# Kernel optimization log

Hardware: AMD Instinct MI355X
Metric: run time of the kernel (lower is better)

## Reference

```python
import jax, jax.numpy as jnp
import numpy as np

KS = 3      # kernel_size
PAD = 1     # zero padding applied to x before sampling
STRIDE = 1  # stride of p_conv and final conv (as written in the repo)


def conv2d(x, w, b=None, stride=1, padding=0):
    out = jax.lax.conv_general_dilated(
        x, w, (stride, stride), [(padding, padding), (padding, padding)],
        dimension_numbers=("NCHW", "OIHW", "NCHW"))
    if b is not None:
        out = out + b[None, :, None, None]
    return out


def setup_inputs() -> dict:
    key = jax.random.key(0)
    k1, k2, k3, k4 = jax.random.split(key, 4)
    bsz, inc, outc, H, W = 4, 64, 128, 128, 128
    N = KS * KS
    x = jax.random.normal(k1, (bsz, inc, H, W), dtype=jnp.float32)
    # p_conv: Conv2d(inc, 2*ks*ks, 3, padding=1) with bias (small weights -> modest offsets)
    w_p = jax.random.normal(k2, (2 * N, inc, 3, 3), dtype=jnp.float32) * 0.02
    b_p = jax.random.normal(k3, (2 * N,), dtype=jnp.float32) * 0.1
    # final conv: Conv2d(inc, outc, ks, stride=stride, bias=None)
    w_conv = jax.random.normal(k4, (outc, inc, KS, KS), dtype=jnp.float32) * 0.05
    return {"x": x, "w_p": w_p, "b_p": b_p, "w_conv": w_conv}


def deform_conv_forward(x, w_p, b_p, w_conv):
    ks, pad, stride = KS, PAD, STRIDE
    offset = conv2d(x, w_p, b_p, stride=stride, padding=1)  # (b, 2N, oh, ow)
    N = offset.shape[1] // 2
    bsz, c, _, _ = x.shape
    oh, ow = offset.shape[2], offset.shape[3]
    xp = jnp.pad(x, ((0, 0), (0, 0), (pad, pad), (pad, pad)))
    Hp, Wp = xp.shape[2], xp.shape[3]

    # p_n: kernel-grid offsets, order matches torch.meshgrid 'ij' then flatten
    r = jnp.arange(-(ks - 1) // 2, (ks - 1) // 2 + 1, dtype=x.dtype)
    pnx, pny = jnp.meshgrid(r, r, indexing="ij")
    p_n = jnp.concatenate([pnx.ravel(), pny.ravel()])[None, :, None, None]  # (1,2N,1,1)

    # p_0: base sampling coordinates (1-indexed into padded image)
    i0 = jnp.arange(1, oh * stride + 1, stride, dtype=x.dtype)
    j0 = jnp.arange(1, ow * stride + 1, stride, dtype=x.dtype)
    p0x = jnp.broadcast_to(i0[:, None], (oh, ow))[None, None]
    p0y = jnp.broadcast_to(j0[None, :], (oh, ow))[None, None]
    p_0 = jnp.concatenate([jnp.tile(p0x, (1, N, 1, 1)), jnp.tile(p0y, (1, N, 1, 1))], axis=1)

    p = (p_0 + p_n + offset).transpose(0, 2, 3, 1)  # (b, oh, ow, 2N)

    q_lt_f = jnp.floor(p)
    q_rb_f = q_lt_f + 1.0

    def clamp_q(q):
        return jnp.concatenate(
            [jnp.clip(q[..., :N], 0, Hp - 1), jnp.clip(q[..., N:], 0, Wp - 1)],
            axis=-1).astype(jnp.int32)

    q_lt = clamp_q(q_lt_f)
    q_rb = clamp_q(q_rb_f)
    q_lb = jnp.concatenate([q_lt[..., :N], q_rb[..., N:]], axis=-1)
    q_rt = jnp.concatenate([q_rb[..., :N], q_lt[..., N:]], axis=-1)

    # clamp p itself (indices are detached in torch; gradients flow only through p here)
    p = jnp.concatenate(
        [jnp.clip(p[..., :N], 0, Hp - 1), jnp.clip(p[..., N:], 0, Wp - 1)], axis=-1)
    px, py = p[..., :N], p[..., N:]

    qf = lambda q: q.astype(x.dtype)
    g_lt = (1 + (qf(q_lt[..., :N]) - px)) * (1 + (qf(q_lt[..., N:]) - py))
    g_rb = (1 - (qf(q_rb[..., :N]) - px)) * (1 - (qf(q_rb[..., N:]) - py))
    g_lb = (1 + (qf(q_lb[..., :N]) - px)) * (1 - (qf(q_lb[..., N:]) - py))
    g_rt = (1 - (qf(q_rt[..., :N]) - px)) * (1 + (qf(q_rt[..., N:]) - py))

    x_flat = xp.reshape(bsz, c, Hp * Wp)

    def get_x_q(q):
        idx = q[..., :N] * Wp + q[..., N:]                     # (b, oh, ow, N)
        idxf = jnp.broadcast_to(idx.reshape(bsz, 1, -1), (bsz, c, oh * ow * N))
        return jnp.take_along_axis(x_flat, idxf, axis=2).reshape(bsz, c, oh, ow, N)

    x_off = (g_lt[:, None] * get_x_q(q_lt) + g_rb[:, None] * get_x_q(q_rb)
             + g_lb[:, None] * get_x_q(q_lb) + g_rt[:, None] * get_x_q(q_rt))

    # _reshape_x_offset: (b,c,oh,ow,ks*ks) -> (b,c,oh*ks,ow*ks)
    x_off = x_off.reshape(bsz, c, oh, ow, ks, ks).transpose(0, 1, 2, 4, 3, 5)
    x_off = x_off.reshape(bsz, c, oh * ks, ow * ks)

    return conv2d(x_off, w_conv, None, stride=stride, padding=0)


def reference(x, w_p, b_p, w_conv):
    return deform_conv_forward(x, w_p, b_p, w_conv)
```

## Files before the change

kernel.cpp:

```cpp
#include <hip/hip_runtime.h>
#include <hip/hip_bf16.h>

#define B_   4
#define IC   64
#define OC   128
#define HH   128
#define WW   128
#define HP   130
#define XOF  384
#define XPAD 388
#define OH2  382

typedef __attribute__((ext_vector_type(4))) float f32x4;
typedef __attribute__((ext_vector_type(8))) __bf16 bf16x8;
typedef __attribute__((ext_vector_type(8))) unsigned short us8;
typedef __attribute__((ext_vector_type(4), aligned(4))) float f32x4u;

__device__ __forceinline__ void gload16(const void* gsrc, void* ldst) {
    __builtin_amdgcn_global_load_lds(
        (const __attribute__((address_space(1))) void*)gsrc,
        (__attribute__((address_space(3))) void*)ldst, 16, 0, 0);
}

#define WAITV(N) asm volatile("s_waitcnt vmcnt(" #N ")" ::: "memory")

__device__ __forceinline__ float bf2f(unsigned short u) {
    union { unsigned int i; float f; } v; v.i = ((unsigned int)u) << 16; return v.f;
}
__device__ __forceinline__ unsigned short f2bf(float f) {
    __hip_bfloat16 h = __float2bfloat16(f);
    return reinterpret_cast<unsigned short&>(h);
}

__global__ __launch_bounds__(256) void prologue(const float* __restrict__ x,
                                                const float* __restrict__ w_p,
                                                const float* __restrict__ b_p,
                                                const float* __restrict__ wc,
                                                float* __restrict__ off,
                                                unsigned short* __restrict__ xt,
                                                unsigned short* __restrict__ Bt) {
    __shared__ __align__(16) char smem[18432];
    int bid = blockIdx.x;
    int tid = threadIdx.x;

    if (bid < 2048) {
        unsigned short (*tile)[34] = (unsigned short(*)[34])smem;
        int xt4 = bid & 3;
        int y   = (bid >> 2) & 127;
        int b   = bid >> 9;
        int x0  = xt4 * 32;

        int xl = tid & 31;
        int c8 = tid >> 5;
#pragma unroll
        for (int it = 0; it < 8; ++it) {
            int c = it * 8 + c8;
            tile[c][xl] = f2bf(x[(((size_t)b * IC + c) * HH + y) * WW + x0 + xl]);
        }
        __syncthreads();
        int c2 = (tid & 31) * 2;
#pragma unroll
        for (int it = 0; it < 4; ++it) {
            int xx = (tid >> 5) + it * 8;
            ushort2 v = { tile[c2][xx], tile[c2 + 1][xx] };
            *(ushort2*)(xt + (((size_t)b * HH + y) * WW + x0 + xx) * IC + c2) = v;
        }
    } else if (bid < 3072) {
        float (*part)[64][18] = (float(*)[64][18])smem;
        int obid = bid - 2048;
        int pxl = tid & 63;
        int icq = tid >> 6;
        int seg = obid & 1;
        int row = obid >> 1;
        int py  = row & 127;
        int b   = row >> 7;
        int px  = seg * 64 + pxl;
        int ic0 = __builtin_amdgcn_readfirstlane(icq << 4);

        float acc[18];
#pragma unroll
        for (int co = 0; co < 18; ++co) acc[co] = 0.f;

        const float* xb = x + ((size_t)b * IC + ic0) * HH * WW;

        for (int ci = 0; ci < 16; ++ci) {
            const float* xc = xb + (size_t)ci * HH * WW;
            float xv[9];
#pragma unroll
            for (int ky = 0; ky < 3; ++ky) {
                int yy = py + ky - 1;
                bool yok = (yy >= 0) && (yy < HH);
#pragma unroll
                for (int kx = 0; kx < 3; ++kx) {
                    int xx = px + kx - 1;
                    bool ok = yok && (xx >= 0) && (xx < WW);
                    xv[ky * 3 + kx] = ok ? xc[yy * WW + xx] : 0.f;
                }
            }
#pragma unroll
            for (int co = 0; co < 18; ++co) {
                const float* wrow = w_p + ((size_t)co * IC + ic0 + ci) * 9;
                f32x4u w0 = *(const f32x4u*)wrow;
                f32x4u w1 = *(const f32x4u*)(wrow + 4);
                float  w8 = wrow[8];
                acc[co] = fmaf(w0.x, xv[0], acc[co]);
                acc[co] = fmaf(w0.y, xv[1], acc[co]);
                acc[co] = fmaf(w0.z, xv[2], acc[co]);
                acc[co] = fmaf(w0.w, xv[3], acc[co]);
                acc[co] = fmaf(w1.x, xv[4], acc[co]);
                acc[co] = fmaf(w1.y, xv[5], acc[co]);
                acc[co] = fmaf(w1.z, xv[6], acc[co]);
                acc[co] = fmaf(w1.w, xv[7], acc[co]);
                acc[co] = fmaf(w8,   xv[8], acc[co]);
            }
        }

#pragma unroll
        for (int co = 0; co < 18; ++co) part[icq][pxl][co] = acc[co];
        __syncthreads();

        for (int co = icq; co < 18; co += 4) {
            float s = b_p[co] + part[0][pxl][co] + part[1][pxl][co]
                              + part[2][pxl][co] + part[3][pxl][co];
            off[((size_t)b * 18 + co) * HH * WW + (size_t)py * WW + px] = s;
        }
    } else {
        int t = (bid - 3072) * 256 + tid;
        if (t < 18 * 4 * 128 * 8) {
            int e  = t & 7;
            int oc = (t >> 3) & 127;
            int kg = (t >> 10) & 3;
            int s  = t >> 12;
            int ic = ((s & 1) << 5) + (kg << 3) + e;
            int kpos = s >> 1;
            int ky = kpos / 3, kx = kpos % 3;
            Bt[t] = f2bf(wc[(((size_t)oc * IC + ic) * 3 + ky) * 3 + kx]);
        }
    }
}

__global__ __launch_bounds__(256) void sample_nhwc(const unsigned short* __restrict__ xt,
                                                   const float* __restrict__ off,
                                                   unsigned short* __restrict__ xoff,
                                                   int b0, int nwg) {
    int orig = blockIdx.x;
    int chunk = nwg >> 3;
    int wg = (orig & 7) * chunk + (orig >> 3);

    int xtile = wg % 12;
    int tmp = wg / 12;
    int yy  = tmp % XOF;
    int bl  = tmp / XOF;
    int b   = b0 + bl;
    int xx0 = xtile * 32;

    int t  = threadIdx.x;
    int xl = t & 31;
    int cg = t >> 5;
    int xx = xx0 + xl;

    int j = xx / 3, kw = xx % 3;
    int i = yy / 3, kh = yy % 3;
    int n = kh * 3 + kw;

    const float* offb = off + (size_t)b * 18 * HH * WW + (size_t)i * WW + j;
    float offr = offb[(size_t)n * HH * WW];
    float offc = offb[(size_t)(n + 9) * HH * WW];

    float pr = (float)(i + kh) + offr;
    float pc = (float)(j + kw) + offc;

    float r0f = floorf(pr), c0f = floorf(pc);
    int r0 = min(max((int)r0f, 0), HP - 1);
    int c0 = min(max((int)c0f, 0), HP - 1);
    int r1 = min(max((int)(r0f + 1.f), 0), HP - 1);
    int c1 = min(max((int)(c0f + 1.f), 0), HP - 1);

    float prc = fminf(fmaxf(pr, 0.f), (float)(HP - 1));
    float pcc = fminf(fmaxf(pc, 0.f), (float)(HP - 1));

    float R0 = 1.f + ((float)r0 - prc);
    float R1 = 1.f - ((float)r1 - prc);
    float C0 = 1.f + ((float)c0 - pcc);
    float C1 = 1.f - ((float)c1 - pcc);

    int rr0 = r0 - 1, cc0 = c0 - 1, rr1 = r1 - 1, cc1 = c1 - 1;
    if (!(rr0 >= 0 && rr0 < HH)) R0 = 0.f;
    if (!(rr1 >= 0 && rr1 < HH)) R1 = 0.f;
    float C0m = (cc0 >= 0 && cc0 < WW) ? C0 : 0.f;
    float C1m = (cc1 >= 0 && cc1 < WW) ? C1 : 0.f;
    int ra0 = min(max(rr0, 0), HH - 1);
    int ra1 = min(max(rr1, 0), HH - 1);
    int ca0 = min(max(cc0, 0), WW - 1);
    int ca1 = min(max(cc1, 0), WW - 1);

    const unsigned short* xb = xt + (size_t)b * HH * WW * IC + cg * 8;
    us8 a  = *(const us8*)(xb + ((size_t)ra0 * WW + ca0) * IC);
    us8 bb = *(const us8*)(xb + ((size_t)ra0 * WW + ca1) * IC);
    us8 cc = *(const us8*)(xb + ((size_t)ra1 * WW + ca0) * IC);
    us8 dd = *(const us8*)(xb + ((size_t)ra1 * WW + ca1) * IC);

    us8 res;
#pragma unroll
    for (int e = 0; e < 8; ++e) {
        float v = R0 * (C0m * bf2f(a[e]) + C1m * bf2f(bb[e])) +
                  R1 * (C0m * bf2f(cc[e]) + C1m * bf2f(dd[e]));
        res[e] = f2bf(v);
    }

    size_t di = ((((size_t)bl * XOF + yy) * 8 + cg) * XPAD + xx) * 8;
    *(us8*)(xoff + di) = res;
}

__global__ __launch_bounds__(256) void conv2_mfma(const unsigned short* __restrict__ xoff,
                                                  const unsigned short* __restrict__ Bt,
                                                  float* __restrict__ out,
                                                  int b0, int nwg) {
    __shared__ __align__(16) char lds[49152];

    int orig = blockIdx.x;
    int q = nwg >> 3, r = nwg & 7;
    int xcd = orig & 7, loc = orig >> 3;
    int wgid = (xcd < r ? xcd * (q + 1) : r * (q + 1) + (xcd - r) * q) + loc;

    int xt  = wgid % 3;
    int tmp = wgid / 3;
    int oy  = tmp % OH2;
    int bl  = tmp / OH2;
    int x0  = xt << 7;

    int tid  = threadIdx.x;
    int wave = tid >> 6, lane = tid & 63;
    int wm = wave >> 1;
    int wn = wave & 1;
    int lr = lane & 15, lc = lane >> 4;

    const char* xb = (const char*)xoff + (size_t)bl * ((size_t)XOF * 8 * XPAD * 16);
    const char* bt = (const char*)Bt;

    f32x4 acc[4][4];
#pragma unroll
    for (int mf = 0; mf < 4; ++mf)
#pragma unroll
        for (int nf = 0; nf < 4; ++nf)
            acc[mf][nf] = (f32x4){0.f, 0.f, 0.f, 0.f};

    auto stageA_full = [&](int abuf, int s6) {
#pragma unroll
        for (int qq = 0; qq < 3; ++qq) {
            int ky  = s6 >> 1;
            int ich = s6 & 1;
            int L   = wave * 3 + qq;
            int cg  = L / 3, seg = L % 3;
            const char* src = xb +
                (((size_t)(oy + ky) * 8 + ich * 4 + cg) * XPAD + x0 + seg * 64 + lane) * 16;
            char* dst = lds + abuf * 12288 + (cg * 192 + seg * 64) * 16;
            gload16(src, dst);
        }
    };
    auto stageB = [&](int t) {
        int s6 = t / 3, kx = t % 3;
        int sB = ((s6 >> 1) * 3 + kx) * 2 + (s6 & 1);
        int buf = t % 3;
        const char* bsrc = bt + (size_t)sB * 8192;
#pragma unroll
        for (int g2 = 0; g2 < 2; ++g2) {
            int g = wave * 2 + g2;
            gload16(bsrc + (size_t)g * 1024 + lane * 16,
                    lds + 24576 + buf * 8192 + g * 1024);
        }
    };

    auto compute = [&](int abuf, int t, int kx) {
        const char* abase = lds + abuf * 12288;
        const char* bbase = lds + 24576 + (t % 3) * 8192;
        bf16x8 af[4], bfr[4];
#pragma unroll
        for (int mf = 0; mf < 4; ++mf)
            af[mf] = *(const bf16x8*)(abase +
                (lc * 192 + wm * 64 + mf * 16 + lr + kx) * 16);
#pragma unroll
        for (int nf = 0; nf < 4; ++nf)
            bfr[nf] = *(const bf16x8*)(bbase +
                (lc * 128 + wn * 64 + nf * 16 + lr) * 16);
        __builtin_amdgcn_s_setprio(1);
#pragma unroll
        for (int mf = 0; mf < 4; ++mf)
#pragma unroll
            for (int nf = 0; nf < 4; ++nf)
                acc[mf][nf] = __builtin_amdgcn_mfma_f32_16x16x32_bf16(
                    af[mf], bfr[nf], acc[mf][nf], 0, 0, 0);
        __builtin_amdgcn_s_setprio(0);
    };

    stageA_full(0, 0);
    stageB(0);
    stageB(1);

#pragma unroll
    for (int t = 0; t < 18; ++t) {
        const int kx = t % 3, s6 = t / 3;
        const int n = (t == 17) ? 0 : ((t % 3 == 1 && t < 15) ? 5 : 2);
        if (n == 0)      { WAITV(0); }
        else if (n == 2) { WAITV(2); }
        else             { WAITV(5); }
        __builtin_amdgcn_s_barrier();
        __builtin_amdgcn_sched_barrier(0);
        if (t + 2 < 18) stageB(t + 2);
        if (kx == 0 && s6 + 1 < 6) stageA_full((s6 & 1) ^ 1, s6 + 1);
        compute(s6 & 1, t, kx);
        __builtin_amdgcn_sched_barrier(0);
    }

    int b = b0 + bl;
#pragma unroll
    for (int mf = 0; mf < 4; ++mf) {
        int ox0 = x0 + wm * 64 + mf * 16 + (lc << 2);
#pragma unroll
        for (int nf = 0; nf < 4; ++nf) {
            int oc = wn * 64 + nf * 16 + lr;
            float* po = out + (((size_t)b * OC + oc) * OH2 + oy) * OH2 + ox0;
            if (ox0 + 3 < OH2) {
                *(f32x4u*)po = acc[mf][nf];
            } else {
#pragma unroll
                for (int rr = 0; rr < 4; ++rr)
                    if (ox0 + rr < OH2) po[rr] = acc[mf][nf][rr];
            }
        }
    }
}

extern "C" void kernel_launch(void* const* d_in, const int* in_sizes, int n_in,
                              void* d_out, int out_size, void* d_ws, size_t ws_size,
                              hipStream_t stream) {
    const float* x      = (const float*)d_in[0];
    const float* w_p    = (const float*)d_in[1];
    const float* b_p    = (const float*)d_in[2];
    const float* w_conv = (const float*)d_in[3];
    float* out = (float*)d_out;

    const size_t offElems = (size_t)B_ * 18 * HH * WW;
    const size_t xtElems  = (size_t)B_ * HH * WW * IC;
    const size_t btElems  = (size_t)18 * 4 * 128 * 8;
    const size_t xofElems = (size_t)XOF * 8 * XPAD * 8;
    const size_t slack    = 16384;

    float* off = (float*)d_ws;
    unsigned short* xtb  = (unsigned short*)(off + offElems);
    unsigned short* Bt   = xtb + xtElems;
    unsigned short* xoff = Bt + btElems;

    const size_t headBytes = offElems * 4 + (xtElems + btElems) * 2;
    const bool allBatch = ws_size >= headBytes + 4 * xofElems * 2 + slack;

    prologue<<<3360, 256, 0, stream>>>(x, w_p, b_p, w_conv, off, xtb, Bt);

    if (allBatch) {
        int snwg = 12 * XOF * B_;
        sample_nhwc<<<snwg, 256, 0, stream>>>(xtb, off, xoff, 0, snwg);
        int cnwg = 3 * OH2 * B_;
        conv2_mfma<<<cnwg, 256, 0, stream>>>(xoff, Bt, out, 0, cnwg);
    } else {
        for (int b = 0; b < B_; ++b) {
            int snwg = 12 * XOF;
            sample_nhwc<<<snwg, 256, 0, stream>>>(xtb, off, xoff, b, snwg);
            int cnwg = 3 * OH2;
            conv2_mfma<<<cnwg, 256, 0, stream>>>(xoff, Bt, out, b, cnwg);
        }
    }
}
```

Baseline: 217.7 us.

## Load conv weights straight to registers and cut per-step LDS barriers

The B (weight) fragments are now loaded from global memory directly into double-buffered registers, instead of being staged through LDS with async global-to-LDS copies. LDS now holds only the double-buffered A tile, with a padded row stride of 194, which shrinks LDS use. The workgroup barrier now runs only when the A buffer switches, once every three k-steps, rather than on every step. This trades shared weight staging for redundant per-wave global/L2 reads of the weights, in exchange for fewer barriers, less LDS traffic and possibly higher occupancy.

```diff
diff --git a/kernel.cpp b/kernel.cpp
--- a/kernel.cpp
+++ b/kernel.cpp
@@ -10,6 +10,7 @@
 #define XOF  384
 #define XPAD 388
 #define OH2  382
+#define PXS  194
 
 typedef __attribute__((ext_vector_type(4))) float f32x4;
 typedef __attribute__((ext_vector_type(8))) __bf16 bf16x8;
@@ -216,7 +217,7 @@
                                                   const unsigned short* __restrict__ Bt,
                                                   float* __restrict__ out,
                                                   int b0, int nwg) {
-    __shared__ __align__(16) char lds[49152];
+    __shared__ __align__(16) char lds[2 * 4 * PXS * 16];
 
     int orig = blockIdx.x;
     int q = nwg >> 3, r = nwg & 7;
@@ -237,6 +238,8 @@
 
     const char* xb = (const char*)xoff + (size_t)bl * ((size_t)XOF * 8 * XPAD * 16);
     const char* bt = (const char*)Bt;
+    const int boff = ((lc * 128) + wn * 64 + lr) * 16;
+    const int ABUF = 4 * PXS * 16;
 
     f32x4 acc[4][4];
 #pragma unroll
@@ -246,43 +249,35 @@
             acc[mf][nf] = (f32x4){0.f, 0.f, 0.f, 0.f};
 
     auto stageA_full = [&](int abuf, int s6) {
+        int ky  = s6 >> 1;
+        int ich = s6 & 1;
 #pragma unroll
         for (int qq = 0; qq < 3; ++qq) {
-            int ky  = s6 >> 1;
-            int ich = s6 & 1;
-            int L   = wave * 3 + qq;
-            int cg  = L / 3, seg = L % 3;
+            int L  = wave * 3 + qq;
+            int cg = L / 3, seg = L % 3;
             const char* src = xb +
                 (((size_t)(oy + ky) * 8 + ich * 4 + cg) * XPAD + x0 + seg * 64 + lane) * 16;
-            char* dst = lds + abuf * 12288 + (cg * 192 + seg * 64) * 16;
+            char* dst = lds + abuf * ABUF + cg * (PXS * 16) + seg * 1024;
             gload16(src, dst);
         }
     };
-    auto stageB = [&](int t) {
+
+    auto loadB = [&](bf16x8* dst, int t) {
         int s6 = t / 3, kx = t % 3;
         int sB = ((s6 >> 1) * 3 + kx) * 2 + (s6 & 1);
-        int buf = t % 3;
-        const char* bsrc = bt + (size_t)sB * 8192;
-#pragma unroll
-        for (int g2 = 0; g2 < 2; ++g2) {
-            int g = wave * 2 + g2;
-            gload16(bsrc + (size_t)g * 1024 + lane * 16,
-                    lds + 24576 + buf * 8192 + g * 1024);
-        }
+        const char* bsrc = bt + (size_t)sB * 8192 + boff;
+#pragma unroll
+        for (int nf = 0; nf < 4; ++nf)
+            dst[nf] = *(const bf16x8*)(bsrc + nf * 256);
     };
 
-    auto compute = [&](int abuf, int t, int kx) {
-        const char* abase = lds + abuf * 12288;
-        const char* bbase = lds + 24576 + (t % 3) * 8192;
-        bf16x8 af[4], bfr[4];
+    auto compute = [&](int abuf, int kx, const bf16x8* bfr) {
+        const char* abase = lds + abuf * ABUF;
+        bf16x8 af[4];
 #pragma unroll
         for (int mf = 0; mf < 4; ++mf)
-            af[mf] = *(const bf16x8*)(abase +
-                (lc * 192 + wm * 64 + mf * 16 + lr + kx) * 16);
-#pragma unroll
-        for (int nf = 0; nf < 4; ++nf)
-            bfr[nf] = *(const bf16x8*)(bbase +
-                (lc * 128 + wn * 64 + nf * 16 + lr) * 16);
+            af[mf] = *(const bf16x8*)(abase + lc * (PXS * 16) +
+                (wm * 64 + mf * 16 + lr + kx) * 16);
         __builtin_amdgcn_s_setprio(1);
 #pragma unroll
         for (int mf = 0; mf < 4; ++mf)
@@ -293,23 +288,30 @@
         __builtin_amdgcn_s_setprio(0);
     };
 
+    bf16x8 bA[4], bB[4];
+
     stageA_full(0, 0);
-    stageB(0);
-    stageB(1);
-
+    loadB(bA, 0);
+    WAITV(4);
+    __builtin_amdgcn_s_barrier();
+    __builtin_amdgcn_sched_barrier(0);
+
+    int abuf = 0;
 #pragma unroll
     for (int t = 0; t < 18; ++t) {
         const int kx = t % 3, s6 = t / 3;
-        const int n = (t == 17) ? 0 : ((t % 3 == 1 && t < 15) ? 5 : 2);
-        if (n == 0)      { WAITV(0); }
-        else if (n == 2) { WAITV(2); }
-        else             { WAITV(5); }
-        __builtin_amdgcn_s_barrier();
-        __builtin_amdgcn_sched_barrier(0);
-        if (t + 2 < 18) stageB(t + 2);
-        if (kx == 0 && s6 + 1 < 6) stageA_full((s6 & 1) ^ 1, s6 + 1);
-        compute(s6 & 1, t, kx);
-        __builtin_amdgcn_sched_barrier(0);
+        if (t + 1 < 18) {
+            if (t & 1) loadB(bA, t + 1);
+            else       loadB(bB, t + 1);
+        }
+        if (kx == 0 && s6 + 1 < 6) stageA_full(abuf ^ 1, s6 + 1);
+        compute(abuf, kx, (t & 1) ? bB : bA);
+        if (kx == 2 && s6 + 1 < 6) {
+            WAITV(4);
+            __builtin_amdgcn_s_barrier();
+            __builtin_amdgcn_sched_barrier(0);
+            abuf ^= 1;
+        }
     }
 
     int b = b0 + bl;
```

New measurement: 222.1 us. 1.02x slower.
